# Kernel tuning notes

Measured on AMD Instinct MI355X. Metric: run time of the kernel, lower is better.

The kernel has to match this reference:

```python
import jax, jax.numpy as jnp
import numpy as np

N, E, F, H, C, G = 100000, 1600000, 128, 64, 40, 2048


def setup_inputs() -> dict:
    key = jax.random.key(0)
    ks = jax.random.split(key, 8)
    x = jax.random.normal(ks[0], (N, F), dtype=jnp.float32)
    edge_index = jax.random.randint(ks[1], (2, E), 0, N, dtype=jnp.int64)
    batch = jnp.sort(jax.random.randint(ks[2], (N,), 0, G, dtype=jnp.int64))
    def glorot(k, shp):
        fan_in, fan_out = shp
        s = jnp.sqrt(2.0 / (fan_in + fan_out))
        return jax.random.normal(k, shp, dtype=jnp.float32) * s
    return {
        "x": x, "edge_index": edge_index, "batch": batch,
        "pre_w": glorot(ks[3], (F, H)), "pre_b": jnp.zeros((H,), jnp.float32),
        "c1_w": glorot(ks[4], (H, H)), "c1_b": jnp.zeros((H,), jnp.float32),
        "n1_g": jnp.ones((H,), jnp.float32), "n1_b": jnp.zeros((H,), jnp.float32),
        "c2_w": glorot(ks[5], (H, H)), "c2_b": jnp.zeros((H,), jnp.float32),
        "n2_g": jnp.ones((H,), jnp.float32), "n2_b": jnp.zeros((H,), jnp.float32),
        "post_w": glorot(ks[6], (H, C)), "post_b": jnp.zeros((C,), jnp.float32),
    }


def _gcn_conv(h, src, dst, deg_isqrt, W, b):
    # GCNConv with self-loops and symmetric D^{-1/2}(A+I)D^{-1/2} normalization.
    hw = h @ W                                        # [N, H]
    coef = deg_isqrt[src] * deg_isqrt[dst]            # [E]
    msg = hw[src] * coef[:, None]                     # gather + scale
    agg = jax.ops.segment_sum(msg, dst, num_segments=N)
    agg = agg + hw * (deg_isqrt * deg_isqrt)[:, None]  # self-loop term
    return agg + b


def _layer_norm(h, g, b, eps=1e-5):
    mu = jnp.mean(h, axis=-1, keepdims=True)
    var = jnp.mean(jnp.square(h - mu), axis=-1, keepdims=True)
    return (h - mu) * jax.lax.rsqrt(var + eps) * g + b


def reference(x, edge_index, batch, pre_w, pre_b, c1_w, c1_b, n1_g, n1_b,
              c2_w, c2_b, n2_g, n2_b, post_w, post_b):
    src, dst = edge_index[0], edge_index[1]
    ones = jnp.ones((E,), dtype=x.dtype)
    deg = jax.ops.segment_sum(ones, dst, num_segments=N) + 1.0  # +1 self-loop
    deg_isqrt = jax.lax.rsqrt(deg)

    h = x @ pre_w + pre_b                              # pre-process MLP
    h1 = jax.nn.relu(_layer_norm(_gcn_conv(h, src, dst, deg_isqrt, c1_w, c1_b), n1_g, n1_b))
    h2 = jax.nn.relu(_layer_norm(_gcn_conv(h1, src, dst, deg_isqrt, c2_w, c2_b), n2_g, n2_b))
    skip = h1 + h2                                     # sum of skip connections
    readout = jax.ops.segment_sum(skip, batch, num_segments=G)  # sum pooling
    return readout @ post_w + post_b                   # [G, C]
```

## Files before the change

### kernel.cpp

```cpp
#include <hip/hip_runtime.h>
#include <hip/hip_fp16.h>

#define NN 100000
#define NE 1600000
#define FIN 128
#define HD 64
#define CO 40
#define NG 2048
#define NSB 196
#define SCAP 9216
#define GCAP 13312
#define CHUNK 4096
#define NSCAT ((NE + CHUNK - 1) / CHUNK)

typedef _Float16 half8 __attribute__((ext_vector_type(8)));
typedef float floatx4 __attribute__((ext_vector_type(4)));

union RowU { float4 f4; __half2 h2[4]; };

__global__ __launch_bounds__(256) void setup_kernel(int* __restrict__ scur,
                                                    float* __restrict__ readout,
                                                    unsigned int* __restrict__ dummy,
                                                    unsigned int* __restrict__ dummy2,
                                                    const float* __restrict__ pre_w,
                                                    const float* __restrict__ pre_b,
                                                    const float* __restrict__ c1_w,
                                                    const float* __restrict__ c2_w,
                                                    _Float16* __restrict__ wth,
                                                    float* __restrict__ beff,
                                                    _Float16* __restrict__ wt2h) {
    int b = blockIdx.x;
    if (b < 512) {
        int gid = b * 256 + threadIdx.x;
        if (gid < NG * HD) readout[gid] = 0.0f;
        if (gid < NSB) scur[gid * 16] = gid * SCAP;
        if (gid < HD / 2) { dummy[gid] = 0u; dummy2[gid] = 0u; }
        return;
    }
    b -= 512;
    if (b < 32) {
        int o = b * 256 + threadIdx.x;
        int r = o >> 6, c = o & 63;
        float acc = 0.0f;
#pragma unroll 8
        for (int k = 0; k < HD; k++) acc = fmaf(pre_w[r * HD + k], c1_w[k * HD + c], acc);
        wth[c * FIN + r] = (_Float16)acc;
    } else if (b == 32) {
        int c = threadIdx.x;
        if (c < HD) {
            float acc = 0.0f;
#pragma unroll 8
            for (int k = 0; k < HD; k++) acc = fmaf(pre_b[k], c1_w[k * HD + c], acc);
            beff[c] = acc;
        }
    } else {
        int o = (b - 33) * 256 + threadIdx.x;
        int r = o >> 6, c = o & 63;
        wt2h[c * HD + r] = (_Float16)c2_w[o];
    }
}

__global__ __launch_bounds__(1024) void scatter_super(const int* __restrict__ src,
                                                      const int* __restrict__ dst,
                                                      int* __restrict__ scur,
                                                      unsigned int* __restrict__ stmp) {
    __shared__ int hist[NSB];
    __shared__ int gbase[NSB];
    int tid = threadIdx.x;
    int e0 = blockIdx.x * CHUNK;
    int d[4], s[4];
    if (tid < NSB) hist[tid] = 0;
    __syncthreads();
#pragma unroll
    for (int r = 0; r < 4; r++) {
        int e = e0 + tid + r * 1024;
        d[r] = -1; s[r] = 0;
        if (e < NE) {
            d[r] = dst[e];
            s[r] = src[e];
            atomicAdd(&hist[d[r] >> 9], 1);
        }
    }
    __syncthreads();
    if (tid < NSB) {
        int c = hist[tid];
        gbase[tid] = (c > 0) ? atomicAdd(&scur[tid * 16], c) : 0;
        hist[tid] = 0;
    }
    __syncthreads();
#pragma unroll
    for (int r = 0; r < 4; r++) {
        if (d[r] >= 0) {
            int b = d[r] >> 9;
            int p = atomicAdd(&hist[b], 1);
            stmp[gbase[b] + p] = ((unsigned int)(d[r] & 511) << 17) | (unsigned int)s[r];
        }
    }
}

__global__ __launch_bounds__(1024) void group_sort(const int* __restrict__ scur,
                                                   const unsigned int* __restrict__ stmp,
                                                   unsigned int* __restrict__ ssrc,
                                                   int* __restrict__ offs,
                                                   int* __restrict__ degn,
                                                   float* __restrict__ di) {
    __shared__ int lh[512];
    __shared__ int sc[512];
    __shared__ int lcur[512];
    int g = blockIdx.x;
    int tid = threadIdx.x;
    int base = g * SCAP;
    int cnt = scur[g * 16] - base;
    if (tid < 512) lh[tid] = 0;
    __syncthreads();
    unsigned int uv[9];
#pragma unroll
    for (int r = 0; r < 9; r++) {
        int i = tid + r * 1024;
        uv[r] = 0xFFFFFFFFu;
        if (i < cnt) {
            uv[r] = stmp[base + i];
            atomicAdd(&lh[uv[r] >> 17], 1);
        }
    }
    __syncthreads();
    int h = 0, pd = 0;
    if (tid < 512) {
        h = lh[tid];
        pd = (h + 7) & ~7;
        sc[tid] = pd;
    }
    __syncthreads();
    for (int off = 1; off < 512; off <<= 1) {
        int v = 0;
        if (tid >= off && tid < 512) v = sc[tid - off];
        __syncthreads();
        if (tid < 512) sc[tid] += v;
        __syncthreads();
    }
    if (tid < 512) {
        int excl = sc[tid] - pd;
        lcur[tid] = excl;
        int node = g * 512 + tid;
        if (node < NN) {
            offs[node] = g * GCAP + excl;
            degn[node] = pd;
            di[node] = rsqrtf((float)h + 1.0f);
        }
        size_t gb = (size_t)g * GCAP;
        for (int q = h; q < pd; q++) ssrc[gb + excl + q] = (unsigned int)NN;
    }
    __syncthreads();
#pragma unroll
    for (int r = 0; r < 9; r++) {
        unsigned int u = uv[r];
        if (u != 0xFFFFFFFFu) {
            int dl = (int)(u >> 17);
            int pos = atomicAdd(&lcur[dl], 1);
            ssrc[(size_t)g * GCAP + pos] = u & 0x1FFFFu;
        }
    }
}

__global__ __launch_bounds__(256, 4) void gemm1_mfma(const float* __restrict__ x,
                                                     const _Float16* __restrict__ wt,
                                                     const float* __restrict__ beff,
                                                     const float* __restrict__ di,
                                                     __half* __restrict__ hws) {
    __shared__ _Float16 wS[64 * 136];
    int tid = threadIdx.x;
    for (int i = tid; i < 1024; i += 256) {
        int n = i >> 4, k0 = (i & 15) * 8;
        *(uint4*)&wS[n * 136 + k0] = ((const uint4*)wt)[i];
    }
    __syncthreads();
    int wv = tid >> 6, lane = tid & 63;
    int l15 = lane & 15, lg = lane >> 4;
    int rbase = blockIdx.x * 64 + wv * 16;
    if (rbase >= NN) return;
    half8 bf[4][4];
#pragma unroll
    for (int ks = 0; ks < 4; ks++)
#pragma unroll
        for (int ns = 0; ns < 4; ns++)
            bf[ks][ns] = *(const half8*)&wS[(ns * 16 + l15) * 136 + ks * 32 + lg * 8];
    floatx4 acc[4];
#pragma unroll
    for (int ns = 0; ns < 4; ns++) acc[ns] = (floatx4){0.f, 0.f, 0.f, 0.f};
    const float* xrow = x + (size_t)(rbase + l15) * FIN;
#pragma unroll
    for (int ks = 0; ks < 4; ks++) {
        float4 lo = *(const float4*)(xrow + ks * 32 + lg * 8);
        float4 hi = *(const float4*)(xrow + ks * 32 + lg * 8 + 4);
        half8 a;
        a[0] = (_Float16)lo.x; a[1] = (_Float16)lo.y; a[2] = (_Float16)lo.z; a[3] = (_Float16)lo.w;
        a[4] = (_Float16)hi.x; a[5] = (_Float16)hi.y; a[6] = (_Float16)hi.z; a[7] = (_Float16)hi.w;
#pragma unroll
        for (int ns = 0; ns < 4; ns++)
            acc[ns] = __builtin_amdgcn_mfma_f32_16x16x32_f16(a, bf[ks][ns], acc[ns], 0, 0, 0);
    }
    int r0 = rbase + lg * 4;
#pragma unroll
    for (int ns = 0; ns < 4; ns++) {
        float be = beff[ns * 16 + l15];
#pragma unroll
        for (int r = 0; r < 4; r++) {
            float dn = di[r0 + r];
            hws[(size_t)(r0 + r) * HD + ns * 16 + l15] = __float2half((acc[ns][r] + be) * dn);
        }
    }
}

__device__ __forceinline__ RowU ldrow(const __half* __restrict__ hws, unsigned int idx, int fp) {
    RowU r;
    r.f4 = ((const float4*)(hws + (size_t)idx * HD))[fp];
    return r;
}

#define LDA8(A, B) { u0 = ldrow(hws, (A).x, fp); u1 = ldrow(hws, (A).y, fp); \
                     u2 = ldrow(hws, (A).z, fp); u3 = ldrow(hws, (A).w, fp); \
                     u4 = ldrow(hws, (B).x, fp); u5 = ldrow(hws, (B).y, fp); \
                     u6 = ldrow(hws, (B).z, fp); u7 = ldrow(hws, (B).w, fp); }
#define LDB8(A, B) { v0 = ldrow(hws, (A).x, fp); v1 = ldrow(hws, (A).y, fp); \
                     v2 = ldrow(hws, (A).z, fp); v3 = ldrow(hws, (A).w, fp); \
                     v4 = ldrow(hws, (B).x, fp); v5 = ldrow(hws, (B).y, fp); \
                     v6 = ldrow(hws, (B).z, fp); v7 = ldrow(hws, (B).w, fp); }
#define ACC4(Q, U) { hacc[Q][0] = __hadd2(hacc[Q][0], (U).h2[0]); \
                     hacc[Q][1] = __hadd2(hacc[Q][1], (U).h2[1]); \
                     hacc[Q][2] = __hadd2(hacc[Q][2], (U).h2[2]); \
                     hacc[Q][3] = __hadd2(hacc[Q][3], (U).h2[3]); }
#define ACCA8() { ACC4(0, u0) ACC4(1, u1) ACC4(2, u2) ACC4(3, u3) \
                  ACC4(0, u4) ACC4(1, u5) ACC4(2, u6) ACC4(3, u7) }
#define ACCB8() { ACC4(0, v0) ACC4(1, v1) ACC4(2, v2) ACC4(3, v3) \
                  ACC4(0, v4) ACC4(1, v5) ACC4(2, v6) ACC4(3, v7) }

__device__ __forceinline__ void gather_node8(const int* __restrict__ offs,
                                             const int* __restrict__ pdeg,
                                             const unsigned int* __restrict__ ssrc,
                                             const __half* __restrict__ hws,
                                             int node, int fp, float acc[8]) {
    int i0 = offs[node];
    int deg = pdeg[node];
    const uint4* ip = (const uint4*)(ssrc + i0);
    __half2 hacc[4][4];
#pragma unroll
    for (int s = 0; s < 4; s++)
#pragma unroll
        for (int t = 0; t < 4; t++) hacc[s][t] = __floats2half2_rn(0.f, 0.f);
    {
        RowU sl = ldrow(hws, (unsigned int)node, fp);
#pragma unroll
        for (int t = 0; t < 4; t++) hacc[0][t] = sl.h2[t];
    }
    int nit = deg >> 3;
    if (nit > 0) {
        RowU u0, u1, u2, u3, u4, u5, u6, u7;
        RowU v0, v1, v2, v3, v4, v5, v6, v7;
        {
            uint4 a = ip[0], b = ip[1];
            LDA8(a, b);
        }
        int it = 1;
        for (; it + 1 < nit; it += 2) {
            uint4 a1 = ip[2 * it], b1 = ip[2 * it + 1];
            LDB8(a1, b1);
            ACCA8();
            uint4 a2 = ip[2 * it + 2], b2 = ip[2 * it + 3];
            LDA8(a2, b2);
            ACCB8();
        }
        if (it < nit) {
            uint4 a1 = ip[2 * it], b1 = ip[2 * it + 1];
            LDB8(a1, b1);
            ACCA8();
            ACCB8();
        } else {
            ACCA8();
        }
    }
#pragma unroll
    for (int t = 0; t < 4; t++) {
        float2 a = __half22float2(hacc[0][t]);
        float2 b = __half22float2(hacc[1][t]);
        float2 c = __half22float2(hacc[2][t]);
        float2 d = __half22float2(hacc[3][t]);
        acc[2 * t]     = (a.x + b.x) + (c.x + d.x);
        acc[2 * t + 1] = (a.y + b.y) + (c.y + d.y);
    }
}

__device__ __forceinline__ void ln8(float v[8], int fp,
                                    const float* __restrict__ g,
                                    const float* __restrict__ bb,
                                    float y[8]) {
    float su = 0.0f;
#pragma unroll
    for (int t = 0; t < 8; t++) su += v[t];
    su += __shfl_xor(su, 1, 64); su += __shfl_xor(su, 2, 64); su += __shfl_xor(su, 4, 64);
    float mu = su * (1.0f / HD);
    float q = 0.0f;
#pragma unroll
    for (int t = 0; t < 8; t++) { float d = v[t] - mu; q += d * d; }
    q += __shfl_xor(q, 1, 64); q += __shfl_xor(q, 2, 64); q += __shfl_xor(q, 4, 64);
    float rstd = rsqrtf(q * (1.0f / HD) + 1e-5f);
    float4 ga = ((const float4*)g)[fp * 2], gb = ((const float4*)g)[fp * 2 + 1];
    float4 ba = ((const float4*)bb)[fp * 2], bc = ((const float4*)bb)[fp * 2 + 1];
    float gv[8] = {ga.x, ga.y, ga.z, ga.w, gb.x, gb.y, gb.z, gb.w};
    float bv[8] = {ba.x, ba.y, ba.z, ba.w, bc.x, bc.y, bc.z, bc.w};
#pragma unroll
    for (int t = 0; t < 8; t++) y[t] = fmaxf((v[t] - mu) * rstd * gv[t] + bv[t], 0.0f);
}

__global__ __launch_bounds__(256, 4) void gather_ln_conv(const int* __restrict__ offs,
                                                         const int* __restrict__ pdeg,
                                                         const unsigned int* __restrict__ ssrc,
                                                         const float* __restrict__ di,
                                                         const __half* __restrict__ hws,
                                                         const float* __restrict__ cb,
                                                         const float* __restrict__ g,
                                                         const float* __restrict__ bb,
                                                         const _Float16* __restrict__ wt2,
                                                         __half* __restrict__ h1out,
                                                         __half* __restrict__ hws2) {
    __shared__ _Float16 wS2[64 * 72];
    __shared__ _Float16 yS[32 * 80];
    int tid = threadIdx.x;
    for (int i = tid; i < 512; i += 256) {
        int n = i >> 3, k0 = (i & 7) * 8;
        *(uint4*)&wS2[n * 72 + k0] = ((const uint4*)wt2)[i];
    }
    int wv = tid >> 6;
    int lane = tid & 63;
    int fp = lane & 7, gg = lane >> 3;
    int l15 = lane & 15, lg = lane >> 4;
    int node = blockIdx.x * 32 + wv * 8 + gg;
    float acc[8];
    gather_node8(offs, pdeg, ssrc, hws, node, fp, acc);
    float4 ca = ((const float4*)cb)[fp * 2], cc = ((const float4*)cb)[fp * 2 + 1];
    float cv[8] = {ca.x, ca.y, ca.z, ca.w, cc.x, cc.y, cc.z, cc.w};
    float dn = di[node];
    float v[8], y[8];
#pragma unroll
    for (int t = 0; t < 8; t++) v[t] = acc[t] * dn + cv[t];
    ln8(v, fp, g, bb, y);
    union U { float4 f4; __half2 h2[4]; } u;
#pragma unroll
    for (int t = 0; t < 4; t++) u.h2[t] = __floats2half2_rn(y[2 * t], y[2 * t + 1]);
    ((float4*)(h1out + (size_t)node * HD))[fp] = u.f4;
    *(float4*)&yS[(wv * 8 + gg) * 80 + fp * 8] = u.f4;
    __syncthreads();
    int tile = wv & 1;
    int nsb = (wv >> 1) * 2;
    half8 bf2[2][2];
#pragma unroll
    for (int ks = 0; ks < 2; ks++)
#pragma unroll
        for (int n = 0; n < 2; n++)
            bf2[ks][n] = *(const half8*)&wS2[((nsb + n) * 16 + l15) * 72 + ks * 32 + lg * 8];
    floatx4 acc2[2];
    acc2[0] = (floatx4){0.f, 0.f, 0.f, 0.f};
    acc2[1] = (floatx4){0.f, 0.f, 0.f, 0.f};
    const _Float16* yrow = &yS[(tile * 16 + l15) * 80];
#pragma unroll
    for (int ks = 0; ks < 2; ks++) {
        half8 a = *(const half8*)(yrow + ks * 32 + lg * 8);
#pragma unroll
        for (int n = 0; n < 2; n++)
            acc2[n] = __builtin_amdgcn_mfma_f32_16x16x32_f16(a, bf2[ks][n], acc2[n], 0, 0, 0);
    }
    int r0 = blockIdx.x * 32 + tile * 16 + lg * 4;
#pragma unroll
    for (int n = 0; n < 2; n++) {
#pragma unroll
        for (int r = 0; r < 4; r++) {
            float d2 = di[r0 + r];
            hws2[(size_t)(r0 + r) * HD + (nsb + n) * 16 + l15] = __float2half(acc2[n][r] * d2);
        }
    }
}

__global__ __launch_bounds__(256, 4) void gather_ln_pool(const int* __restrict__ offs,
                                                         const int* __restrict__ pdeg,
                                                         const unsigned int* __restrict__ ssrc,
                                                         const float* __restrict__ di,
                                                         const __half* __restrict__ hws,
                                                         const float* __restrict__ cb,
                                                         const float* __restrict__ g,
                                                         const float* __restrict__ bb,
                                                         const __half* __restrict__ h1,
                                                         const int* __restrict__ batch,
                                                         float* __restrict__ readout) {
    __shared__ float ls[32][65];
    __shared__ int lb[32];
    int wv = threadIdx.x >> 6;
    int lane = threadIdx.x & 63;
    int fp = lane & 7, gg = lane >> 3;
    int node = blockIdx.x * 32 + wv * 8 + gg;
    float acc[8];
    gather_node8(offs, pdeg, ssrc, hws, node, fp, acc);
    float4 ca = ((const float4*)cb)[fp * 2], cc = ((const float4*)cb)[fp * 2 + 1];
    float cv[8] = {ca.x, ca.y, ca.z, ca.w, cc.x, cc.y, cc.z, cc.w};
    float dn = di[node];
    float v[8], y[8];
#pragma unroll
    for (int t = 0; t < 8; t++) v[t] = acc[t] * dn + cv[t];
    ln8(v, fp, g, bb, y);
    union U { float4 f4; __half2 h2[4]; } u;
    u.f4 = ((const float4*)(h1 + (size_t)node * HD))[fp];
    int row = wv * 8 + gg;
#pragma unroll
    for (int t = 0; t < 4; t++) {
        float2 p = __half22float2(u.h2[t]);
        ls[row][fp * 8 + 2 * t]     = y[2 * t] + p.x;
        ls[row][fp * 8 + 2 * t + 1] = y[2 * t + 1] + p.y;
    }
    if (fp == 0) lb[row] = batch[node];
    int r0 = wv * 8;
    int bu = lb[r0];
    bool uni = true;
#pragma unroll
    for (int r = 1; r < 8; r++) uni = uni && (lb[r0 + r] == bu);
    int f = lane;
    if (uni) {
        float s2 = 0.0f;
#pragma unroll
        for (int r = 0; r < 8; r++) s2 += ls[r0 + r][f];
        atomicAdd(&readout[(size_t)bu * HD + f], s2);
    } else {
        float s2 = ls[r0][f];
        int bprev = lb[r0];
#pragma unroll
        for (int r = 1; r < 8; r++) {
            int bn = lb[r0 + r];
            if (bn == bprev) {
                s2 += ls[r0 + r][f];
            } else {
                atomicAdd(&readout[(size_t)bprev * HD + f], s2);
                s2 = ls[r0 + r][f];
                bprev = bn;
            }
        }
        atomicAdd(&readout[(size_t)bprev * HD + f], s2);
    }
}

__global__ __launch_bounds__(256) void out_gemm(const float* __restrict__ r,
                                                const float* __restrict__ w,
                                                const float* __restrict__ b,
                                                float* __restrict__ out) {
    __shared__ float lw[HD * CO];
    for (int i = threadIdx.x; i < HD * CO; i += 256) lw[i] = w[i];
    __syncthreads();
    int grp = blockIdx.x * 4 + (threadIdx.x >> 6);
    int c = threadIdx.x & 63;
    if (grp >= NG || c >= CO) return;
    const float* rr = r + (size_t)grp * HD;
    float acc = b[c];
#pragma unroll 8
    for (int k = 0; k < HD; k++) acc = fmaf(rr[k], lw[k * CO + c], acc);
    out[(size_t)grp * CO + c] = acc;
}

extern "C" void kernel_launch(void* const* d_in, const int* in_sizes, int n_in,
                              void* d_out, int out_size, void* d_ws, size_t ws_size,
                              hipStream_t stream) {
    const float* x      = (const float*)d_in[0];
    const int*   ei     = (const int*)d_in[1];
    const int*   batch  = (const int*)d_in[2];
    const float* pre_w  = (const float*)d_in[3];
    const float* pre_b  = (const float*)d_in[4];
    const float* c1_w   = (const float*)d_in[5];
    const float* c1_b   = (const float*)d_in[6];
    const float* n1_g   = (const float*)d_in[7];
    const float* n1_b   = (const float*)d_in[8];
    const float* c2_w   = (const float*)d_in[9];
    const float* c2_b   = (const float*)d_in[10];
    const float* n2_g   = (const float*)d_in[11];
    const float* n2_b   = (const float*)d_in[12];
    const float* post_w = (const float*)d_in[13];
    const float* post_b = (const float*)d_in[14];

    const int* src = ei;
    const int* dst = ei + NE;

    char* p = (char*)d_ws;
    int*          scur    = (int*)p;          p += (size_t)NSB * 16 * 4;
    int*          offs    = (int*)p;          p += (size_t)NN * 4;
    int*          degn    = (int*)p;          p += (size_t)NN * 4;
    float*        di      = (float*)p;        p += (size_t)NN * 4;
    _Float16*     wth     = (_Float16*)p;     p += (size_t)FIN * HD * 2;
    _Float16*     wt2h    = (_Float16*)p;     p += (size_t)HD * HD * 2;
    float*        beff    = (float*)p;        p += 256;
    unsigned int* stmp    = (unsigned int*)p; p += (size_t)NSB * SCAP * 4;
    unsigned int* ssrc    = (unsigned int*)p; p += (size_t)NSB * GCAP * 4;
    float*        readout = (float*)p;        p += (size_t)NG * HD * 4;
    __half*       hws     = (__half*)p;       p += (size_t)(NN + 8) * HD * 2;
    __half*       hws2    = (__half*)p;       p += (size_t)(NN + 8) * HD * 2;
    __half*       h1      = (__half*)p;       p += (size_t)NN * HD * 2;

    setup_kernel<<<561, 256, 0, stream>>>(scur, readout,
                                          (unsigned int*)(hws + (size_t)NN * HD),
                                          (unsigned int*)(hws2 + (size_t)NN * HD),
                                          pre_w, pre_b, c1_w, c2_w, wth, beff, wt2h);

    scatter_super<<<NSCAT, 1024, 0, stream>>>(src, dst, scur, stmp);
    group_sort<<<NSB, 1024, 0, stream>>>(scur, stmp, ssrc, offs, degn, di);

    gemm1_mfma<<<(NN + 63) / 64, 256, 0, stream>>>(x, wth, beff, di, hws);

    gather_ln_conv<<<NN / 32, 256, 0, stream>>>(offs, degn, ssrc, di, hws,
                                                c1_b, n1_g, n1_b, wt2h, h1, hws2);

    gather_ln_pool<<<NN / 32, 256, 0, stream>>>(offs, degn, ssrc, di, hws2,
                                                c2_b, n2_g, n2_b, h1, batch, readout);

    out_gemm<<<(NG + 3) / 4, 256, 0, stream>>>(readout, post_w, post_b, (float*)d_out);
}
```

Before: 229.3 us.

## Bucket nodes by padded degree so gather waves process similar-degree nodes

```diff
diff --git a/kernel.cpp b/kernel.cpp
--- a/kernel.cpp
+++ b/kernel.cpp
@@ -103,15 +103,19 @@
                                                    unsigned int* __restrict__ ssrc,
                                                    int* __restrict__ offs,
                                                    int* __restrict__ degn,
-                                                   float* __restrict__ di) {
+                                                   float* __restrict__ di,
+                                                   int* __restrict__ perm) {
     __shared__ int lh[512];
     __shared__ int sc[512];
     __shared__ int lcur[512];
+    __shared__ int ch[16];
+    __shared__ int cbase[16];
     int g = blockIdx.x;
     int tid = threadIdx.x;
     int base = g * SCAP;
     int cnt = scur[g * 16] - base;
     if (tid < 512) lh[tid] = 0;
+    if (tid < 16) ch[tid] = 0;
     __syncthreads();
     unsigned int uv[9];
 #pragma unroll
@@ -124,11 +128,15 @@
         }
     }
     __syncthreads();
-    int h = 0, pd = 0;
+    int h = 0, pd = 0, cls = 0, cpos = 0;
     if (tid < 512) {
         h = lh[tid];
         pd = (h + 7) & ~7;
         sc[tid] = pd;
+        if (g * 512 + tid < NN) {
+            cls = pd >> 3; if (cls > 15) cls = 15;
+            cpos = atomicAdd(&ch[cls], 1);
+        }
     }
     __syncthreads();
     for (int off = 1; off < 512; off <<= 1) {
@@ -150,7 +158,16 @@
         size_t gb = (size_t)g * GCAP;
         for (int q = h; q < pd; q++) ssrc[gb + excl + q] = (unsigned int)NN;
     }
-    __syncthreads();
+    if (tid == 0) {
+        int run = 0;
+#pragma unroll
+        for (int i = 0; i < 16; i++) { cbase[i] = run; run += ch[i]; }
+    }
+    __syncthreads();
+    if (tid < 512) {
+        int node = g * 512 + tid;
+        if (node < NN) perm[g * 512 + cbase[cls] + cpos] = node;
+    }
 #pragma unroll
     for (int r = 0; r < 9; r++) {
         unsigned int u = uv[r];
@@ -311,7 +328,8 @@
     for (int t = 0; t < 8; t++) y[t] = fmaxf((v[t] - mu) * rstd * gv[t] + bv[t], 0.0f);
 }
 
-__global__ __launch_bounds__(256, 4) void gather_ln_conv(const int* __restrict__ offs,
+__global__ __launch_bounds__(256, 4) void gather_ln_conv(const int* __restrict__ perm,
+                                                         const int* __restrict__ offs,
                                                          const int* __restrict__ pdeg,
                                                          const unsigned int* __restrict__ ssrc,
                                                          const float* __restrict__ di,
@@ -324,6 +342,7 @@
                                                          __half* __restrict__ hws2) {
     __shared__ _Float16 wS2[64 * 72];
     __shared__ _Float16 yS[32 * 80];
+    __shared__ int pnS[32];
     int tid = threadIdx.x;
     for (int i = tid; i < 512; i += 256) {
         int n = i >> 3, k0 = (i & 7) * 8;
@@ -333,7 +352,8 @@
     int lane = tid & 63;
     int fp = lane & 7, gg = lane >> 3;
     int l15 = lane & 15, lg = lane >> 4;
-    int node = blockIdx.x * 32 + wv * 8 + gg;
+    int node = perm[blockIdx.x * 32 + wv * 8 + gg];
+    if (fp == 0) pnS[wv * 8 + gg] = node;
     float acc[8];
     gather_node8(offs, pdeg, ssrc, hws, node, fp, acc);
     float4 ca = ((const float4*)cb)[fp * 2], cc = ((const float4*)cb)[fp * 2 + 1];
@@ -368,18 +388,18 @@
         for (int n = 0; n < 2; n++)
             acc2[n] = __builtin_amdgcn_mfma_f32_16x16x32_f16(a, bf2[ks][n], acc2[n], 0, 0, 0);
     }
-    int r0 = blockIdx.x * 32 + tile * 16 + lg * 4;
-#pragma unroll
-    for (int n = 0; n < 2; n++) {
-#pragma unroll
-        for (int r = 0; r < 4; r++) {
-            float d2 = di[r0 + r];
-            hws2[(size_t)(r0 + r) * HD + (nsb + n) * 16 + l15] = __float2half(acc2[n][r] * d2);
-        }
-    }
-}
-
-__global__ __launch_bounds__(256, 4) void gather_ln_pool(const int* __restrict__ offs,
+#pragma unroll
+    for (int r = 0; r < 4; r++) {
+        int nodeR = pnS[tile * 16 + lg * 4 + r];
+        float d2 = di[nodeR];
+#pragma unroll
+        for (int n = 0; n < 2; n++)
+            hws2[(size_t)nodeR * HD + (nsb + n) * 16 + l15] = __float2half(acc2[n][r] * d2);
+    }
+}
+
+__global__ __launch_bounds__(256, 4) void gather_ln_pool(const int* __restrict__ perm,
+                                                         const int* __restrict__ offs,
                                                          const int* __restrict__ pdeg,
                                                          const unsigned int* __restrict__ ssrc,
                                                          const float* __restrict__ di,
@@ -395,7 +415,7 @@
     int wv = threadIdx.x >> 6;
     int lane = threadIdx.x & 63;
     int fp = lane & 7, gg = lane >> 3;
-    int node = blockIdx.x * 32 + wv * 8 + gg;
+    int node = perm[blockIdx.x * 32 + wv * 8 + gg];
     float acc[8];
     gather_node8(offs, pdeg, ssrc, hws, node, fp, acc);
     float4 ca = ((const float4*)cb)[fp * 2], cc = ((const float4*)cb)[fp * 2 + 1];
@@ -488,6 +508,7 @@
     int*          offs    = (int*)p;          p += (size_t)NN * 4;
     int*          degn    = (int*)p;          p += (size_t)NN * 4;
     float*        di      = (float*)p;        p += (size_t)NN * 4;
+    int*          perm    = (int*)p;          p += (size_t)NN * 4;
     _Float16*     wth     = (_Float16*)p;     p += (size_t)FIN * HD * 2;
     _Float16*     wt2h    = (_Float16*)p;     p += (size_t)HD * HD * 2;
     float*        beff    = (float*)p;        p += 256;
@@ -504,14 +525,14 @@
                                           pre_w, pre_b, c1_w, c2_w, wth, beff, wt2h);
 
     scatter_super<<<NSCAT, 1024, 0, stream>>>(src, dst, scur, stmp);
-    group_sort<<<NSB, 1024, 0, stream>>>(scur, stmp, ssrc, offs, degn, di);
+    group_sort<<<NSB, 1024, 0, stream>>>(scur, stmp, ssrc, offs, degn, di, perm);
 
     gemm1_mfma<<<(NN + 63) / 64, 256, 0, stream>>>(x, wth, beff, di, hws);
 
-    gather_ln_conv<<<NN / 32, 256, 0, stream>>>(offs, degn, ssrc, di, hws,
+    gather_ln_conv<<<NN / 32, 256, 0, stream>>>(perm, offs, degn, ssrc, di, hws,
                                                 c1_b, n1_g, n1_b, wt2h, h1, hws2);
 
-    gather_ln_pool<<<NN / 32, 256, 0, stream>>>(offs, degn, ssrc, di, hws2,
+    gather_ln_pool<<<NN / 32, 256, 0, stream>>>(perm, offs, degn, ssrc, di, hws2,
                                                 c2_b, n2_g, n2_b, h1, batch, readout);
 
     out_gemm<<<(NG + 3) / 4, 256, 0, stream>>>(readout, post_w, post_b, (float*)d_out);
```

Result: no change. 231.2 us (+0.8%).
